# Optimization experiments

Hardware: AMD Instinct MI355X
Metric: run time of the kernel (lower is better)

## Reference

```python
import jax, jax.numpy as jnp
import numpy as np

B, K = 262144, 128

def setup_inputs() -> dict:
    key = jax.random.key(0)
    k1, k2, k3 = jax.random.split(key, 3)
    logits = jax.random.normal(k1, (B, K), dtype=jnp.float32)
    labels = jax.random.randint(k2, (B,), 0, K, dtype=jnp.int32)
    # guarantee every bin's risk set {j: labels_j >= k} is non-empty
    labels = labels.at[0].set(K - 1)
    events = jax.random.randint(k3, (B,), 0, 2, dtype=jnp.int32)
    return {"logits": logits, "labels": labels, "events": events}

def reference(logits, labels, events):
    Bn, Kn = logits.shape
    ev = (events == 1)
    evf = ev.astype(logits.dtype)
    # logits at each sample's own bin: f(x_i, t_{label_i})
    own = jnp.take_along_axis(logits, labels[:, None], axis=1)[:, 0]  # (B,)
    # per-bin event counts and numerators via scatter-add (segment sum)
    n_ev = jnp.zeros((Kn,), logits.dtype).at[labels].add(evf)          # (K,)
    numer = jnp.zeros((Kn,), logits.dtype).at[labels].add(evf * own)   # (K,)
    # risk set R_k = {j : labels_j >= k}; masked per-column logsumexp
    risk_mask = labels[:, None] >= jnp.arange(Kn, dtype=labels.dtype)[None, :]  # (B,K)
    masked = jnp.where(risk_mask, logits, -jnp.inf)
    denom_log = jax.nn.logsumexp(masked, axis=0)                       # (K,)
    terms = jnp.where(n_ev > 0, numer - n_ev * denom_log, jnp.zeros((), logits.dtype))
    n_events_total = jnp.maximum(evf.sum(), jnp.ones((), logits.dtype))
    return -terms.sum() / n_events_total
```

## Files before the change

kernel.cpp:

```cpp
#include <hip/hip_runtime.h>
#include <math.h>

#define KBINS 128
#define NTHR  256

__global__ __launch_bounds__(NTHR) void cox_main(
    const float* __restrict__ logits, const int* __restrict__ labels,
    const int* __restrict__ events, float* __restrict__ part_denom,
    int* __restrict__ part_hist, float* __restrict__ part_s1,
    int* __restrict__ part_ev, int B, int nblk)
{
    __shared__ float dsum[8][KBINS];
    __shared__ int   hsum[8][KBINS];
    __shared__ float s1sh[8];
    __shared__ int   evsh[8];

    const int t    = threadIdx.x;
    const int wave = t >> 6;
    const int lane = t & 63;
    const int half = lane >> 5;
    const int l32  = lane & 31;
    const int hid  = wave * 2 + half;
    const int c0   = l32 << 2;

    float sa0 = 0.f, sa1 = 0.f, sa2 = 0.f, sa3 = 0.f;
    int   h0 = 0, h1 = 0, h2 = 0, h3 = 0;
    float accOwn = 0.f;
    int   accEv  = 0;

    const float4* __restrict__ lg4 = reinterpret_cast<const float4*>(logits);
    const int rowsPerIter = nblk * 8;

    #pragma unroll 2
    for (int r = blockIdx.x * 8 + hid; r < B; r += rowsPerIter) {
        const float4 v  = lg4[(size_t)r * (KBINS / 4) + l32];
        const int   lab = labels[r];
        const int   ev  = events[r];
        const float e0 = __expf(v.x);
        const float e1 = __expf(v.y);
        const float e2 = __expf(v.z);
        const float e3 = __expf(v.w);
        if (lab >= c0    ) sa0 += e0;
        if (lab >= c0 + 1) sa1 += e1;
        if (lab >= c0 + 2) sa2 += e2;
        if (lab >= c0 + 3) sa3 += e3;
        if (ev) {
            if      (lab == c0    ) { accOwn += v.x; h0++; }
            else if (lab == c0 + 1) { accOwn += v.y; h1++; }
            else if (lab == c0 + 2) { accOwn += v.z; h2++; }
            else if (lab == c0 + 3) { accOwn += v.w; h3++; }
            if (l32 == 0) accEv++;
        }
    }

    dsum[hid][c0    ] = sa0;  hsum[hid][c0    ] = h0;
    dsum[hid][c0 + 1] = sa1;  hsum[hid][c0 + 1] = h1;
    dsum[hid][c0 + 2] = sa2;  hsum[hid][c0 + 2] = h2;
    dsum[hid][c0 + 3] = sa3;  hsum[hid][c0 + 3] = h3;

    for (int off = 16; off; off >>= 1)
        accOwn += __shfl_down(accOwn, off, 32);
    if (l32 == 0) { s1sh[hid] = accOwn; evsh[hid] = accEv; }
    __syncthreads();

    if (t < KBINS) {
        float d = 0.f; int h = 0;
        #pragma unroll
        for (int i = 0; i < 8; ++i) { d += dsum[i][t]; h += hsum[i][t]; }
        const size_t o = (size_t)t * nblk + blockIdx.x;
        part_denom[o] = d;
        part_hist[o]  = h;
    }
    if (t == 0) {
        float s1 = 0.f; int e = 0;
        #pragma unroll
        for (int i = 0; i < 8; ++i) { s1 += s1sh[i]; e += evsh[i]; }
        part_s1[blockIdx.x] = s1;
        part_ev[blockIdx.x] = e;
    }
}

__global__ __launch_bounds__(256) void cox_fin1(
    const float* __restrict__ part_denom, const int* __restrict__ part_hist,
    const float* __restrict__ part_s1, const int* __restrict__ part_ev,
    double* __restrict__ term, int nblk)
{
    const int k = blockIdx.x;
    const int t = threadIdx.x;
    __shared__ double ds[256];
    __shared__ long   hs[256];

    double d = 0.0;
    long   h = 0;
    if (k < KBINS) {
        const float* pd = part_denom + (size_t)k * nblk;
        const int*   ph = part_hist  + (size_t)k * nblk;
        for (int b = t; b < nblk; b += 256) { d += (double)pd[b]; h += ph[b]; }
    } else {
        for (int b = t; b < nblk; b += 256) { d += (double)part_s1[b]; h += part_ev[b]; }
    }
    ds[t] = d; hs[t] = h;
    __syncthreads();
    for (int off = 128; off; off >>= 1) {
        if (t < off) { ds[t] += ds[t + off]; hs[t] += hs[t + off]; }
        __syncthreads();
    }
    if (t == 0) {
        if (k < KBINS) term[k] = (hs[0] > 0) ? (double)hs[0] * log(ds[0]) : 0.0;
        else { term[KBINS] = ds[0]; term[KBINS + 1] = (double)hs[0]; }
    }
}

__global__ __launch_bounds__(128) void cox_fin2(
    const double* __restrict__ term, float* __restrict__ out)
{
    const int t = threadIdx.x;
    double v = term[t];
    for (int off = 32; off; off >>= 1)
        v += __shfl_down(v, off, 64);
    __shared__ double w[2];
    if ((t & 63) == 0) w[t >> 6] = v;
    __syncthreads();
    if (t == 0) {
        const double s2   = w[0] + w[1];
        const double s1   = term[KBINS];
        const double ne   = term[KBINS + 1];
        const double ntot = ne > 1.0 ? ne : 1.0;
        out[0] = (float)((s2 - s1) / ntot);
    }
}

extern "C" void kernel_launch(void* const* d_in, const int* in_sizes, int n_in,
                              void* d_out, int out_size, void* d_ws, size_t ws_size,
                              hipStream_t stream) {
    const float* logits = (const float*)d_in[0];
    const int*   labels = (const int*)d_in[1];
    const int*   events = (const int*)d_in[2];
    const int B = in_sizes[1];

    int nblk = 2048;
    auto need = [](size_t nb) {
        return nb * KBINS * 4 * 2
             + nb * 8
             + (KBINS + 2) * 8 + 64;
    };
    while (nblk > 64 && need((size_t)nblk) > ws_size) nblk >>= 1;

    char* ws = (char*)d_ws;
    float*  part_denom = (float*)ws;
    int*    part_hist  = (int*)(ws + (size_t)nblk * KBINS * 4);
    float*  part_s1    = (float*)(ws + (size_t)2 * nblk * KBINS * 4);
    int*    part_ev    = (int*)(ws + (size_t)2 * nblk * KBINS * 4 + (size_t)nblk * 4);
    double* term       = (double*)(ws + (size_t)2 * nblk * KBINS * 4 + (size_t)2 * nblk * 4);

    cox_main<<<nblk, NTHR, 0, stream>>>(logits, labels, events,
                                        part_denom, part_hist, part_s1, part_ev,
                                        B, nblk);
    cox_fin1<<<KBINS + 1, 256, 0, stream>>>(part_denom, part_hist,
                                            part_s1, part_ev, term, nblk);
    cox_fin2<<<1, 128, 0, stream>>>(term, (float*)d_out);
}
```

Baseline: 201.6 us.

## Fuse final reduction into fin kernel via atomics and last-block pattern, double grid

Removes the third kernel launch by having each finalize block atomically add its term into double accumulators, with the last block (detected via an atomic counter) writing the output. Accumulators are zeroed inside the main kernel. The main grid is also raised from 2048 to 4096 blocks, which doubles the partial buffers and the work in the finalize reductions. The atomic accumulation order is nondeterministic, and one launch is saved at the cost of atomics and a larger partials pass.

```diff
diff --git a/kernel.cpp b/kernel.cpp
--- a/kernel.cpp
+++ b/kernel.cpp
@@ -8,7 +8,8 @@
     const float* __restrict__ logits, const int* __restrict__ labels,
     const int* __restrict__ events, float* __restrict__ part_denom,
     int* __restrict__ part_hist, float* __restrict__ part_s1,
-    int* __restrict__ part_ev, int B, int nblk)
+    int* __restrict__ part_ev, double* __restrict__ acc,
+    unsigned* __restrict__ cnt, int B, int nblk)
 {
     __shared__ float dsum[8][KBINS];
     __shared__ int   hsum[8][KBINS];
@@ -22,6 +23,11 @@
     const int l32  = lane & 31;
     const int hid  = wave * 2 + half;
     const int c0   = l32 << 2;
+
+    if (blockIdx.x == 0) {
+        if (t < 4) acc[t] = 0.0;
+        if (t == 0) *cnt = 0u;
+    }
 
     float sa0 = 0.f, sa1 = 0.f, sa2 = 0.f, sa3 = 0.f;
     int   h0 = 0, h1 = 0, h2 = 0, h3 = 0;
@@ -80,10 +86,11 @@
     }
 }
 
-__global__ __launch_bounds__(256) void cox_fin1(
+__global__ __launch_bounds__(256) void cox_fin(
     const float* __restrict__ part_denom, const int* __restrict__ part_hist,
     const float* __restrict__ part_s1, const int* __restrict__ part_ev,
-    double* __restrict__ term, int nblk)
+    double* __restrict__ acc, unsigned* __restrict__ cnt,
+    float* __restrict__ out, int nblk)
 {
     const int k = blockIdx.x;
     const int t = threadIdx.x;
@@ -105,28 +112,22 @@
         if (t < off) { ds[t] += ds[t + off]; hs[t] += hs[t + off]; }
         __syncthreads();
     }
+
     if (t == 0) {
-        if (k < KBINS) term[k] = (hs[0] > 0) ? (double)hs[0] * log(ds[0]) : 0.0;
-        else { term[KBINS] = ds[0]; term[KBINS + 1] = (double)hs[0]; }
-    }
-}
-
-__global__ __launch_bounds__(128) void cox_fin2(
-    const double* __restrict__ term, float* __restrict__ out)
-{
-    const int t = threadIdx.x;
-    double v = term[t];
-    for (int off = 32; off; off >>= 1)
-        v += __shfl_down(v, off, 64);
-    __shared__ double w[2];
-    if ((t & 63) == 0) w[t >> 6] = v;
-    __syncthreads();
-    if (t == 0) {
-        const double s2   = w[0] + w[1];
-        const double s1   = term[KBINS];
-        const double ne   = term[KBINS + 1];
-        const double ntot = ne > 1.0 ? ne : 1.0;
-        out[0] = (float)((s2 - s1) / ntot);
+        if (k < KBINS) {
+            if (hs[0] > 0) atomicAdd(&acc[0], (double)hs[0] * log(ds[0]));
+        } else {
+            atomicAdd(&acc[1], ds[0]);
+            atomicAdd(&acc[2], (double)hs[0]);
+        }
+        __threadfence();
+        const unsigned old = atomicAdd(cnt, 1u);
+        if (old == (unsigned)KBINS) {
+            const double s2 = atomicAdd(&acc[0], 0.0);
+            const double s1 = atomicAdd(&acc[1], 0.0);
+            const double ne = atomicAdd(&acc[2], 0.0);
+            out[0] = (float)((s2 - s1) / (ne > 1.0 ? ne : 1.0));
+        }
     }
 }
 
@@ -138,25 +139,26 @@
     const int*   events = (const int*)d_in[2];
     const int B = in_sizes[1];
 
-    int nblk = 2048;
+    int nblk = 4096;
     auto need = [](size_t nb) {
         return nb * KBINS * 4 * 2
              + nb * 8
-             + (KBINS + 2) * 8 + 64;
+             + 4 * 8 + 8 + 64;
     };
     while (nblk > 64 && need((size_t)nblk) > ws_size) nblk >>= 1;
 
     char* ws = (char*)d_ws;
-    float*  part_denom = (float*)ws;
-    int*    part_hist  = (int*)(ws + (size_t)nblk * KBINS * 4);
-    float*  part_s1    = (float*)(ws + (size_t)2 * nblk * KBINS * 4);
-    int*    part_ev    = (int*)(ws + (size_t)2 * nblk * KBINS * 4 + (size_t)nblk * 4);
-    double* term       = (double*)(ws + (size_t)2 * nblk * KBINS * 4 + (size_t)2 * nblk * 4);
+    float*    part_denom = (float*)ws;
+    int*      part_hist  = (int*)(ws + (size_t)nblk * KBINS * 4);
+    float*    part_s1    = (float*)(ws + (size_t)2 * nblk * KBINS * 4);
+    int*      part_ev    = (int*)(ws + (size_t)2 * nblk * KBINS * 4 + (size_t)nblk * 4);
+    double*   acc        = (double*)(ws + (size_t)2 * nblk * KBINS * 4 + (size_t)2 * nblk * 4);
+    unsigned* cnt        = (unsigned*)(acc + 4);
 
     cox_main<<<nblk, NTHR, 0, stream>>>(logits, labels, events,
                                         part_denom, part_hist, part_s1, part_ev,
-                                        B, nblk);
-    cox_fin1<<<KBINS + 1, 256, 0, stream>>>(part_denom, part_hist,
-                                            part_s1, part_ev, term, nblk);
-    cox_fin2<<<1, 128, 0, stream>>>(term, (float*)d_out);
+                                        acc, cnt, B, nblk);
+    cox_fin<<<KBINS + 1, 256, 0, stream>>>(part_denom, part_hist,
+                                           part_s1, part_ev, acc, cnt,
+                                           (float*)d_out, nblk);
 }
```

New measurement: 207.9 us. 1.03x slower.
